# Kernel optimization log

Measured on AMD Instinct MI355X. Metric: run time of the kernel, lower is better.

## Reference

```python
import jax, jax.numpy as jnp
import numpy as np

B, T, D, H, E = 4, 2048, 768, 3072, 8


def setup_inputs() -> dict:
    key = jax.random.key(0)
    ks = jax.random.split(key, 7)
    s_d = 1.0 / np.sqrt(D)
    s_h = 1.0 / np.sqrt(H)
    return {
        "x": jax.random.normal(ks[0], (B, T, D), dtype=jnp.float32),
        # gate: Linear(D, E). (Original inits to zero; random here for nontrivial routing.)
        "Wg": jax.random.normal(ks[1], (E, D), dtype=jnp.float32) * s_d,
        "bg": jax.random.normal(ks[2], (E,), dtype=jnp.float32) * 0.01,
        # stacked expert MLPs: Linear(D,H) -> GELU(exact) -> Linear(H,D)
        "W1": jax.random.normal(ks[3], (E, D, H), dtype=jnp.float32) * s_d,
        "b1": jax.random.normal(ks[4], (E, H), dtype=jnp.float32) * s_d,
        "W2": jax.random.normal(ks[5], (E, H, D), dtype=jnp.float32) * s_h,
        "b2": jax.random.normal(ks[6], (E, D), dtype=jnp.float32) * s_h,
    }


def reference(x, Wg, bg, W1, b1, W2, b2):
    b, t, d = x.shape
    xf = x.reshape(-1, d)                      # [N, D]
    n = xf.shape[0]
    logits = xf @ Wg.T + bg                    # [N, E]
    probs = jax.nn.softmax(logits, axis=-1)
    top2_vals, top2_idx = jax.lax.top_k(probs, 2)  # [N, 2]
    # combine weights: cw[n, e] = top2 prob if expert e is in token n's top-2 else 0
    cw = jnp.zeros((n, Wg.shape[0]), dtype=x.dtype)
    cw = cw.at[jnp.arange(n)[:, None], top2_idx].set(top2_vals)
    # per-expert MLP on all tokens (zero combine weight kills non-routed experts)
    h = jax.nn.gelu(jnp.einsum('nd,edh->neh', xf, W1) + b1[None], approximate=False)
    y = jnp.einsum('neh,ehd->ned', h, W2) + b2[None]   # [N, E, D]
    out = jnp.einsum('ne,ned->nd', cw, y)
    return out.reshape(b, t, d)
```

## Files before the change

kernel.cpp:

```cpp
#include <hip/hip_runtime.h>
#include <hip/hip_bf16.h>
#include <math.h>

#define E_EXPERTS 8
#define D_DIM 768
#define H_DIM 3072
#define N_TOK 8192
#define SLOTS (2 * N_TOK)
#define SCAT_BLOCKS 32
#define MB_L 20

typedef unsigned short ushort_t;
typedef __attribute__((ext_vector_type(8))) __bf16 bf16x8;
typedef __attribute__((ext_vector_type(4))) float f32x4;

__device__ __forceinline__ unsigned short f2bf(float f) {
    unsigned int u = __float_as_uint(f);
    unsigned int r = (u + 0x7FFFu + ((u >> 16) & 1u)) >> 16;
    return (unsigned short)r;
}

__device__ __forceinline__ void gload_lds16(const void* g, void* l) {
    __builtin_amdgcn_global_load_lds(
        (const __attribute__((address_space(1))) unsigned int*)g,
        (__attribute__((address_space(3))) unsigned int*)l, 16, 0, 0);
}


__global__ void transpose_conv_kernel(const float* __restrict__ src, ushort_t* __restrict__ dst,
                                      int R, int C) {
    __shared__ float tile[64][65];
    int e = blockIdx.z;
    const float* S = src + (size_t)e * R * C;
    ushort_t* Dp = dst + (size_t)e * R * C;
    int c0 = blockIdx.x * 64, r0 = blockIdx.y * 64;
    int tx = threadIdx.x & 15, ty = threadIdx.x >> 4;
#pragma unroll
    for (int p = 0; p < 4; p++) {
        float4 v = *(const float4*)&S[(size_t)(r0 + ty + 16 * p) * C + c0 + tx * 4];
        tile[ty + 16 * p][tx * 4 + 0] = v.x;
        tile[ty + 16 * p][tx * 4 + 1] = v.y;
        tile[ty + 16 * p][tx * 4 + 2] = v.z;
        tile[ty + 16 * p][tx * 4 + 3] = v.w;
    }
    __syncthreads();
#pragma unroll
    for (int p = 0; p < 4; p++) {
        int cc = ty + 16 * p;
        int rr = tx * 4;
        ushort4 o;
        o.x = f2bf(tile[rr + 0][cc]);
        o.y = f2bf(tile[rr + 1][cc]);
        o.z = f2bf(tile[rr + 2][cc]);
        o.w = f2bf(tile[rr + 3][cc]);
        *(ushort4*)&Dp[(size_t)(c0 + cc) * R + r0 + rr] = o;
    }
}


__global__ void gate_kernel(const float* __restrict__ x, const float* __restrict__ Wg,
                            const float* __restrict__ bg, ushort_t* __restrict__ xb,
                            int* __restrict__ top_idx, float* __restrict__ top_w) {
    int w = threadIdx.x >> 6, lane = threadIdx.x & 63;
    int t = blockIdx.x * 4 + w;
    if (t >= N_TOK) return;
    const float* xr = x + (size_t)t * D_DIM;
    float xs[12];
#pragma unroll
    for (int j = 0; j < 12; j++) xs[j] = xr[lane + 64 * j];
#pragma unroll
    for (int j = 0; j < 12; j++) xb[(size_t)t * D_DIM + lane + 64 * j] = f2bf(xs[j]);
    float pr[8];
#pragma unroll
    for (int ee = 0; ee < 8; ee++) {
        const float* wr = Wg + ee * D_DIM;
        float p = 0.f;
#pragma unroll
        for (int j = 0; j < 12; j++) p += xs[j] * wr[lane + 64 * j];
#pragma unroll
        for (int o = 32; o > 0; o >>= 1) p += __shfl_xor(p, o);
        pr[ee] = p + bg[ee];
    }
    float mx = pr[0];
#pragma unroll
    for (int ee = 1; ee < 8; ee++) mx = fmaxf(mx, pr[ee]);
    float s = 0.f;
#pragma unroll
    for (int ee = 0; ee < 8; ee++) { pr[ee] = expf(pr[ee] - mx); s += pr[ee]; }
    float inv = 1.f / s;
#pragma unroll
    for (int ee = 0; ee < 8; ee++) pr[ee] *= inv;
    int i0 = 0;
#pragma unroll
    for (int ee = 1; ee < 8; ee++) if (pr[ee] > pr[i0]) i0 = ee;
    int i1 = -1;
#pragma unroll
    for (int ee = 0; ee < 8; ee++) {
        if (ee == i0) continue;
        if (i1 < 0 || pr[ee] > pr[i1]) i1 = ee;
    }
    if (lane == 0) {
        top_idx[2 * t] = i0;
        top_idx[2 * t + 1] = i1;
        top_w[2 * t] = pr[i0];
        top_w[2 * t + 1] = pr[i1];
    }
}

__global__ void hist_kernel(const int* __restrict__ top_idx, int* __restrict__ bc) {
    __shared__ int h[E_EXPERTS];
    if (threadIdx.x < E_EXPERTS) h[threadIdx.x] = 0;
    __syncthreads();
    int t = blockIdx.x * 256 + threadIdx.x;
    atomicAdd(&h[top_idx[2 * t]], 1);
    atomicAdd(&h[top_idx[2 * t + 1]], 1);
    __syncthreads();
    if (threadIdx.x < E_EXPERTS) bc[blockIdx.x * E_EXPERTS + threadIdx.x] = h[threadIdx.x];
}

__global__ void scan_kernel(const int* __restrict__ bc, int* __restrict__ counts,
                            int* __restrict__ offsets, int* __restrict__ base) {
    int tid = threadIdx.x;
    if (tid < E_EXPERTS) {
        int acc = 0;
        for (int b = 0; b < SCAT_BLOCKS; b++) {
            base[b * E_EXPERTS + tid] = acc;
            acc += bc[b * E_EXPERTS + tid];
        }
        counts[tid] = acc;
    }
    __syncthreads();
    if (tid == 0) {
        int acc = 0;
        for (int e = 0; e < E_EXPERTS; e++) { offsets[e] = acc; acc += counts[e]; }
    }
    __syncthreads();
    if (tid < E_EXPERTS) {
        int o = offsets[tid];
        for (int b = 0; b < SCAT_BLOCKS; b++) base[b * E_EXPERTS + tid] += o;
    }
}

__global__ void scatter_kernel(const int* __restrict__ top_idx, const float* __restrict__ top_w,
                               const int* __restrict__ base, int* __restrict__ perm,
                               float* __restrict__ wgt, int* __restrict__ tok2slot) {
    __shared__ int cur[E_EXPERTS];
    if (threadIdx.x < E_EXPERTS) cur[threadIdx.x] = 0;
    __syncthreads();
    int t = blockIdx.x * 256 + threadIdx.x;
#pragma unroll
    for (int sl = 0; sl < 2; sl++) {
        int ee = top_idx[2 * t + sl];
        int p = atomicAdd(&cur[ee], 1);
        int s = base[blockIdx.x * E_EXPERTS + ee] + p;
        perm[s] = t;
        wgt[s] = top_w[2 * t + sl];
        tok2slot[2 * t + sl] = s;
    }
}

__global__ void combine_kernel(const float* __restrict__ y, const int* __restrict__ tok2slot,
                               float* __restrict__ out) {
    int idx = blockIdx.x * blockDim.x + threadIdx.x;
    int stride = gridDim.x * blockDim.x;
    const int QR = D_DIM / 4;
    for (int i = idx; i < N_TOK * QR; i += stride) {
        int t = i / QR, d4 = i - t * QR;
        int s0 = tok2slot[2 * t], s1 = tok2slot[2 * t + 1];
        float4 a = ((const float4*)(y + (size_t)s0 * D_DIM))[d4];
        float4 b = ((const float4*)(y + (size_t)s1 * D_DIM))[d4];
        float4 o;
        o.x = a.x + b.x; o.y = a.y + b.y; o.z = a.z + b.z; o.w = a.w + b.w;
        ((float4*)(out + (size_t)t * D_DIM))[d4] = o;
    }
}

template <int MODE>
__global__ __launch_bounds__(256, 3) void moe_gemm_kernel(
    const ushort_t* __restrict__ A, const ushort_t* __restrict__ BT,
    const float* __restrict__ bias, const int* __restrict__ offsets,
    const int* __restrict__ counts, const int* __restrict__ perm,
    const float* __restrict__ wgt, ushort_t* __restrict__ Hout, float* __restrict__ Y) {
    constexpr int K = (MODE == 0) ? D_DIM : H_DIM;
    constexpr int N = (MODE == 0) ? H_DIM : D_DIM;
    constexpr int KT = K / 32;
    constexpr int NB = N / 128;

    const int wgid = blockIdx.x;
    const int c = wgid & 7;
    const int r = wgid >> 3;
    const int mb = r % MB_L;
    const int q = r / MB_L;
    const int g = q * 8 + c;
    const int e = g / NB;
    const int nb = g % NB;

    const int ne = counts[e];
    const int m0 = mb * 128;
    if (m0 >= ne) return;
    const int n0 = nb * 128;
    const int base = offsets[e];
    const ushort_t* Bt = BT + (size_t)e * ((size_t)N * K);

    __shared__ alignas(16) ushort_t As[3 * 128 * 32];
    __shared__ alignas(16) ushort_t Bs[3 * 128 * 32];

    const int tid = threadIdx.x;
    const int lane = tid & 63;
    const int w = tid >> 6;
    const int wm = w >> 1, wn = w & 1;
    const int lr = lane & 15;
    const int gq = lane >> 4;

    int lds_dst[2];
    int a_src[2], b_src[2];
#pragma unroll
    for (int i = 0; i < 2; i++) {
        int s = 2 * w + i;
        int row = s * 16 + (lane >> 2);
        int lg = ((lane & 3) - (row >> 1)) & 3;
        int rcl = min(m0 + row, ne - 1);
        int arow = (MODE == 0) ? perm[base + rcl] : (base + rcl);
        a_src[i] = arow * K + lg * 8;
        b_src[i] = (n0 + row) * K + lg * 8;
        lds_dst[i] = s * 512;
    }

    auto stage = [&](int tt, int bi) {
#pragma unroll
        for (int i = 0; i < 2; i++) {
            gload_lds16(A + (size_t)a_src[i] + (size_t)tt * 32, &As[bi * 4096 + lds_dst[i]]);
            gload_lds16(Bt + (size_t)b_src[i] + (size_t)tt * 32, &Bs[bi * 4096 + lds_dst[i]]);
        }
    };

    f32x4 acc[4][4];
#pragma unroll
    for (int i = 0; i < 4; i++)
#pragma unroll
        for (int j = 0; j < 4; j++) acc[i][j] = (f32x4){0.f, 0.f, 0.f, 0.f};

    stage(0, 0);
    stage(1, 1);
    asm volatile("s_waitcnt vmcnt(4)" ::: "memory");
    __builtin_amdgcn_s_barrier();

    int cur = 0;
    for (int t = 0; t < KT; ++t) {
        int sb = cur + 2; if (sb >= 3) sb -= 3;
        if (t + 2 < KT) stage(t + 2, sb);
        bf16x8 af[4], bfr[4];
#pragma unroll
        for (int f = 0; f < 4; f++) {
            int Ra = wm * 64 + f * 16 + lr;
            int Rb = wn * 64 + f * 16 + lr;
            af[f]  = *(const bf16x8*)&As[cur * 4096 + Ra * 32 + (((gq + (Ra >> 1)) & 3) << 3)];
            bfr[f] = *(const bf16x8*)&Bs[cur * 4096 + Rb * 32 + (((gq + (Rb >> 1)) & 3) << 3)];
        }
        asm volatile("s_waitcnt lgkmcnt(0)" ::: "memory");
        __builtin_amdgcn_s_setprio(1);
#pragma unroll
        for (int fm = 0; fm < 4; fm++)
#pragma unroll
            for (int fc = 0; fc < 4; fc++)
                acc[fm][fc] = __builtin_amdgcn_mfma_f32_16x16x32_bf16(
                    af[fm], bfr[fc], acc[fm][fc], 0, 0, 0);
        __builtin_amdgcn_s_setprio(0);
        if (t + 2 < KT) asm volatile("s_waitcnt vmcnt(4)" ::: "memory");
        else            asm volatile("s_waitcnt vmcnt(0)" ::: "memory");
        __builtin_amdgcn_s_barrier();
        cur = (cur == 2) ? 0 : cur + 1;
    }

    const int rg0 = gq * 4;
#pragma unroll
    for (int fr = 0; fr < 4; fr++) {
#pragma unroll
        for (int fc = 0; fc < 4; fc++) {
            int cn = n0 + wn * 64 + fc * 16 + lr;
            float bi = bias[e * N + cn];
            f32x4 v = acc[fr][fc];
#pragma unroll
            for (int rg = 0; rg < 4; rg++) {
                int rm = m0 + wm * 64 + fr * 16 + rg0 + rg;
                if (rm < ne) {
                    if (MODE == 0) {
                        float xv = v[rg] + bi;
                        float u = xv * 1.5957691216f * __builtin_fmaf(0.044715f * xv, xv, 1.0f);
                        float gl = xv / (1.f + __expf(-u));
                        Hout[(size_t)(base + rm) * H_DIM + cn] = f2bf(gl);
                    } else {
                        int s = base + rm;
                        float wv = wgt[s];
                        Y[(size_t)s * D_DIM + cn] = wv * (v[rg] + bi);
                    }
                }
            }
        }
    }
}


extern "C" void kernel_launch(void* const* d_in, const int* in_sizes, int n_in,
                              void* d_out, int out_size, void* d_ws, size_t ws_size,
                              hipStream_t stream) {
    const float* x  = (const float*)d_in[0];
    const float* Wg = (const float*)d_in[1];
    const float* bg = (const float*)d_in[2];
    const float* W1 = (const float*)d_in[3];
    const float* b1 = (const float*)d_in[4];
    const float* W2 = (const float*)d_in[5];
    const float* b2 = (const float*)d_in[6];
    float* out = (float*)d_out;

    char* p = (char*)d_ws;
    ushort_t* xb  = (ushort_t*)p; p += (size_t)N_TOK * D_DIM * 2;
    ushort_t* W1T = (ushort_t*)p; p += (size_t)E_EXPERTS * H_DIM * D_DIM * 2;
    ushort_t* W2T = (ushort_t*)p; p += (size_t)E_EXPERTS * D_DIM * H_DIM * 2;
    ushort_t* Hb  = (ushort_t*)p; p += (size_t)SLOTS * H_DIM * 2;
    int*   top_idx = (int*)p;   p += (size_t)N_TOK * 2 * 4;
    float* top_w   = (float*)p; p += (size_t)N_TOK * 2 * 4;
    int*   perm    = (int*)p;   p += (size_t)SLOTS * 4;
    float* wgt     = (float*)p; p += (size_t)SLOTS * 4;
    int*   t2s     = (int*)p;   p += (size_t)SLOTS * 4;
    int*   bc      = (int*)p;   p += SCAT_BLOCKS * E_EXPERTS * 4;
    int*   basep   = (int*)p;   p += SCAT_BLOCKS * E_EXPERTS * 4;
    int*   counts  = (int*)p;   p += 64;
    int*   offsets = (int*)p;   p += 64;
    float* y = (float*)d_ws;

    gate_kernel<<<N_TOK / 4, 256, 0, stream>>>(x, Wg, bg, xb, top_idx, top_w);
    transpose_conv_kernel<<<dim3(H_DIM / 64, D_DIM / 64, E_EXPERTS), 256, 0, stream>>>(W1, W1T, D_DIM, H_DIM);
    transpose_conv_kernel<<<dim3(D_DIM / 64, H_DIM / 64, E_EXPERTS), 256, 0, stream>>>(W2, W2T, H_DIM, D_DIM);
    hist_kernel<<<SCAT_BLOCKS, 256, 0, stream>>>(top_idx, bc);
    scan_kernel<<<1, 64, 0, stream>>>(bc, counts, offsets, basep);
    scatter_kernel<<<SCAT_BLOCKS, 256, 0, stream>>>(top_idx, top_w, basep, perm, wgt, t2s);
    moe_gemm_kernel<0><<<8 * MB_L * (H_DIM / 128), 256, 0, stream>>>(
        xb, W1T, b1, offsets, counts, perm, wgt, Hb, nullptr);
    moe_gemm_kernel<1><<<8 * MB_L * (D_DIM / 128), 256, 0, stream>>>(
        Hb, W2T, b2, offsets, counts, perm, wgt, nullptr, y);
    combine_kernel<<<2048, 256, 0, stream>>>(y, t2s, out);
}
```

Measured before the change: 395.4 us.

## Widen MoE GEMM tiles to 128x256 with 8 waves and add nontemporal stores

```diff
diff --git a/kernel.cpp b/kernel.cpp
--- a/kernel.cpp
+++ b/kernel.cpp
@@ -167,16 +167,15 @@
     for (int i = idx; i < N_TOK * QR; i += stride) {
         int t = i / QR, d4 = i - t * QR;
         int s0 = tok2slot[2 * t], s1 = tok2slot[2 * t + 1];
-        float4 a = ((const float4*)(y + (size_t)s0 * D_DIM))[d4];
-        float4 b = ((const float4*)(y + (size_t)s1 * D_DIM))[d4];
-        float4 o;
-        o.x = a.x + b.x; o.y = a.y + b.y; o.z = a.z + b.z; o.w = a.w + b.w;
-        ((float4*)(out + (size_t)t * D_DIM))[d4] = o;
+        f32x4 a = __builtin_nontemporal_load((const f32x4*)(y + (size_t)s0 * D_DIM) + d4);
+        f32x4 b = __builtin_nontemporal_load((const f32x4*)(y + (size_t)s1 * D_DIM) + d4);
+        f32x4 o = a + b;
+        __builtin_nontemporal_store(o, (f32x4*)(out + (size_t)t * D_DIM) + d4);
     }
 }
 
 template <int MODE>
-__global__ __launch_bounds__(256, 3) void moe_gemm_kernel(
+__global__ __launch_bounds__(512, 4) void moe_gemm_kernel(
     const ushort_t* __restrict__ A, const ushort_t* __restrict__ BT,
     const float* __restrict__ bias, const int* __restrict__ offsets,
     const int* __restrict__ counts, const int* __restrict__ perm,
@@ -184,7 +183,7 @@
     constexpr int K = (MODE == 0) ? D_DIM : H_DIM;
     constexpr int N = (MODE == 0) ? H_DIM : D_DIM;
     constexpr int KT = K / 32;
-    constexpr int NB = N / 128;
+    constexpr int NB = N / 256;
 
     const int wgid = blockIdx.x;
     const int c = wgid & 7;
@@ -198,40 +197,44 @@
     const int ne = counts[e];
     const int m0 = mb * 128;
     if (m0 >= ne) return;
-    const int n0 = nb * 128;
+    const int n0 = nb * 256;
     const int base = offsets[e];
     const ushort_t* Bt = BT + (size_t)e * ((size_t)N * K);
 
     __shared__ alignas(16) ushort_t As[3 * 128 * 32];
-    __shared__ alignas(16) ushort_t Bs[3 * 128 * 32];
+    __shared__ alignas(16) ushort_t Bs[3 * 256 * 32];
 
     const int tid = threadIdx.x;
     const int lane = tid & 63;
     const int w = tid >> 6;
-    const int wm = w >> 1, wn = w & 1;
+    const int wm = w >> 2, wn = w & 3;
     const int lr = lane & 15;
     const int gq = lane >> 4;
 
-    int lds_dst[2];
-    int a_src[2], b_src[2];
-#pragma unroll
-    for (int i = 0; i < 2; i++) {
-        int s = 2 * w + i;
-        int row = s * 16 + (lane >> 2);
-        int lg = ((lane & 3) - (row >> 1)) & 3;
-        int rcl = min(m0 + row, ne - 1);
+    const int lrow = lane >> 2;
+    const int lpg = lane & 3;
+    int a_src, b_src[2];
+    {
+        int rowA = w * 16 + lrow;
+        int lgA = (lpg - (rowA >> 1)) & 3;
+        int rcl = min(m0 + rowA, ne - 1);
         int arow = (MODE == 0) ? perm[base + rcl] : (base + rcl);
-        a_src[i] = arow * K + lg * 8;
-        b_src[i] = (n0 + row) * K + lg * 8;
-        lds_dst[i] = s * 512;
+        a_src = arow * K + lgA * 8;
+#pragma unroll
+        for (int i = 0; i < 2; i++) {
+            int s = 2 * w + i;
+            int rowB = s * 16 + lrow;
+            int lgB = (lpg - (rowB >> 1)) & 3;
+            b_src[i] = (n0 + rowB) * K + lgB * 8;
+        }
     }
 
     auto stage = [&](int tt, int bi) {
-#pragma unroll
-        for (int i = 0; i < 2; i++) {
-            gload_lds16(A + (size_t)a_src[i] + (size_t)tt * 32, &As[bi * 4096 + lds_dst[i]]);
-            gload_lds16(Bt + (size_t)b_src[i] + (size_t)tt * 32, &Bs[bi * 4096 + lds_dst[i]]);
-        }
+        gload_lds16(A + (size_t)a_src + (size_t)tt * 32, &As[bi * 4096 + w * 512]);
+#pragma unroll
+        for (int i = 0; i < 2; i++)
+            gload_lds16(Bt + (size_t)b_src[i] + (size_t)tt * 32,
+                        &Bs[bi * 8192 + (2 * w + i) * 512]);
     };
 
     f32x4 acc[4][4];
@@ -242,7 +245,7 @@
 
     stage(0, 0);
     stage(1, 1);
-    asm volatile("s_waitcnt vmcnt(4)" ::: "memory");
+    asm volatile("s_waitcnt vmcnt(3)" ::: "memory");
     __builtin_amdgcn_s_barrier();
 
     int cur = 0;
@@ -255,7 +258,7 @@
             int Ra = wm * 64 + f * 16 + lr;
             int Rb = wn * 64 + f * 16 + lr;
             af[f]  = *(const bf16x8*)&As[cur * 4096 + Ra * 32 + (((gq + (Ra >> 1)) & 3) << 3)];
-            bfr[f] = *(const bf16x8*)&Bs[cur * 4096 + Rb * 32 + (((gq + (Rb >> 1)) & 3) << 3)];
+            bfr[f] = *(const bf16x8*)&Bs[cur * 8192 + Rb * 32 + (((gq + (Rb >> 1)) & 3) << 3)];
         }
         asm volatile("s_waitcnt lgkmcnt(0)" ::: "memory");
         __builtin_amdgcn_s_setprio(1);
@@ -266,7 +269,7 @@
                 acc[fm][fc] = __builtin_amdgcn_mfma_f32_16x16x32_bf16(
                     af[fm], bfr[fc], acc[fm][fc], 0, 0, 0);
         __builtin_amdgcn_s_setprio(0);
-        if (t + 2 < KT) asm volatile("s_waitcnt vmcnt(4)" ::: "memory");
+        if (t + 2 < KT) asm volatile("s_waitcnt vmcnt(3)" ::: "memory");
         else            asm volatile("s_waitcnt vmcnt(0)" ::: "memory");
         __builtin_amdgcn_s_barrier();
         cur = (cur == 2) ? 0 : cur + 1;
@@ -288,11 +291,13 @@
                         float xv = v[rg] + bi;
                         float u = xv * 1.5957691216f * __builtin_fmaf(0.044715f * xv, xv, 1.0f);
                         float gl = xv / (1.f + __expf(-u));
-                        Hout[(size_t)(base + rm) * H_DIM + cn] = f2bf(gl);
+                        __builtin_nontemporal_store(
+                            f2bf(gl), &Hout[(size_t)(base + rm) * H_DIM + cn]);
                     } else {
                         int s = base + rm;
                         float wv = wgt[s];
-                        Y[(size_t)s * D_DIM + cn] = wv * (v[rg] + bi);
+                        __builtin_nontemporal_store(
+                            wv * (v[rg] + bi), &Y[(size_t)s * D_DIM + cn]);
                     }
                 }
             }
@@ -335,9 +340,9 @@
     hist_kernel<<<SCAT_BLOCKS, 256, 0, stream>>>(top_idx, bc);
     scan_kernel<<<1, 64, 0, stream>>>(bc, counts, offsets, basep);
     scatter_kernel<<<SCAT_BLOCKS, 256, 0, stream>>>(top_idx, top_w, basep, perm, wgt, t2s);
-    moe_gemm_kernel<0><<<8 * MB_L * (H_DIM / 128), 256, 0, stream>>>(
+    moe_gemm_kernel<0><<<8 * MB_L * (H_DIM / 256), 512, 0, stream>>>(
         xb, W1T, b1, offsets, counts, perm, wgt, Hb, nullptr);
-    moe_gemm_kernel<1><<<8 * MB_L * (D_DIM / 128), 256, 0, stream>>>(
+    moe_gemm_kernel<1><<<8 * MB_L * (D_DIM / 256), 512, 0, stream>>>(
         Hb, W2T, b2, offsets, counts, perm, wgt, nullptr, y);
     combine_kernel<<<2048, 256, 0, stream>>>(y, t2s, out);
 }
```

After: 378.7 us. -4.2%, faster.

## Use single-buffered 64-wide K tiles with XOR swizzle in MoE GEMM

Applied to the files above, without the earlier changes.

```diff
diff --git a/kernel.cpp b/kernel.cpp
--- a/kernel.cpp
+++ b/kernel.cpp
@@ -167,11 +167,10 @@
     for (int i = idx; i < N_TOK * QR; i += stride) {
         int t = i / QR, d4 = i - t * QR;
         int s0 = tok2slot[2 * t], s1 = tok2slot[2 * t + 1];
-        float4 a = ((const float4*)(y + (size_t)s0 * D_DIM))[d4];
-        float4 b = ((const float4*)(y + (size_t)s1 * D_DIM))[d4];
-        float4 o;
-        o.x = a.x + b.x; o.y = a.y + b.y; o.z = a.z + b.z; o.w = a.w + b.w;
-        ((float4*)(out + (size_t)t * D_DIM))[d4] = o;
+        f32x4 a = __builtin_nontemporal_load((const f32x4*)(y + (size_t)s0 * D_DIM) + d4);
+        f32x4 b = __builtin_nontemporal_load((const f32x4*)(y + (size_t)s1 * D_DIM) + d4);
+        f32x4 o = a + b;
+        __builtin_nontemporal_store(o, (f32x4*)(out + (size_t)t * D_DIM) + d4);
     }
 }
 
@@ -183,7 +182,7 @@
     const float* __restrict__ wgt, ushort_t* __restrict__ Hout, float* __restrict__ Y) {
     constexpr int K = (MODE == 0) ? D_DIM : H_DIM;
     constexpr int N = (MODE == 0) ? H_DIM : D_DIM;
-    constexpr int KT = K / 32;
+    constexpr int KT = K / 64;
     constexpr int NB = N / 128;
 
     const int wgid = blockIdx.x;
@@ -202,77 +201,72 @@
     const int base = offsets[e];
     const ushort_t* Bt = BT + (size_t)e * ((size_t)N * K);
 
-    __shared__ alignas(16) ushort_t As[3 * 128 * 32];
-    __shared__ alignas(16) ushort_t Bs[3 * 128 * 32];
+    __shared__ alignas(16) ushort_t As[128 * 64];
+    __shared__ alignas(16) ushort_t Bs[128 * 64];
 
     const int tid = threadIdx.x;
     const int lane = tid & 63;
     const int w = tid >> 6;
     const int wm = w >> 1, wn = w & 1;
     const int lr = lane & 15;
-    const int gq = lane >> 4;
-
-    int lds_dst[2];
-    int a_src[2], b_src[2];
-#pragma unroll
-    for (int i = 0; i < 2; i++) {
-        int s = 2 * w + i;
-        int row = s * 16 + (lane >> 2);
-        int lg = ((lane & 3) - (row >> 1)) & 3;
+    const int lk8 = lane >> 4;
+
+    const int trow = tid >> 3;
+    const int sg8 = (((tid & 7) ^ (trow & 7)) * 8);
+    int a_off[4], b_off[4];
+#pragma unroll
+    for (int i = 0; i < 4; i++) {
+        int row = i * 32 + trow;
         int rcl = min(m0 + row, ne - 1);
         int arow = (MODE == 0) ? perm[base + rcl] : (base + rcl);
-        a_src[i] = arow * K + lg * 8;
-        b_src[i] = (n0 + row) * K + lg * 8;
-        lds_dst[i] = s * 512;
-    }
-
-    auto stage = [&](int tt, int bi) {
-#pragma unroll
-        for (int i = 0; i < 2; i++) {
-            gload_lds16(A + (size_t)a_src[i] + (size_t)tt * 32, &As[bi * 4096 + lds_dst[i]]);
-            gload_lds16(Bt + (size_t)b_src[i] + (size_t)tt * 32, &Bs[bi * 4096 + lds_dst[i]]);
+        a_off[i] = arow * K + sg8;
+        b_off[i] = (n0 + row) * K + sg8;
+    }
+
+    auto stage = [&](int tt) {
+#pragma unroll
+        for (int i = 0; i < 4; i++)
+            gload_lds16(A + (size_t)a_off[i] + (size_t)tt * 64, &As[(i * 256 + w * 64) * 8]);
+#pragma unroll
+        for (int i = 0; i < 4; i++)
+            gload_lds16(Bt + (size_t)b_off[i] + (size_t)tt * 64, &Bs[(i * 256 + w * 64) * 8]);
+    };
+
+    f32x4 acc[4][4];
+#pragma unroll
+    for (int i = 0; i < 4; i++)
+#pragma unroll
+        for (int j = 0; j < 4; j++) acc[i][j] = (f32x4){0.f, 0.f, 0.f, 0.f};
+
+    const int cg0 = ((0 * 4 + lk8) ^ (lr & 7)) << 3;
+    const int cg1 = ((1 * 4 + lk8) ^ (lr & 7)) << 3;
+
+    stage(0);
+    for (int t = 0; t < KT; ++t) {
+        __syncthreads();
+        bf16x8 bfr[4][2];
+#pragma unroll
+        for (int fc = 0; fc < 4; fc++) {
+            int Rb = (wn * 64 + fc * 16 + lr) * 64;
+            bfr[fc][0] = *(const bf16x8*)&Bs[Rb + cg0];
+            bfr[fc][1] = *(const bf16x8*)&Bs[Rb + cg1];
         }
-    };
-
-    f32x4 acc[4][4];
-#pragma unroll
-    for (int i = 0; i < 4; i++)
-#pragma unroll
-        for (int j = 0; j < 4; j++) acc[i][j] = (f32x4){0.f, 0.f, 0.f, 0.f};
-
-    stage(0, 0);
-    stage(1, 1);
-    asm volatile("s_waitcnt vmcnt(4)" ::: "memory");
-    __builtin_amdgcn_s_barrier();
-
-    int cur = 0;
-    for (int t = 0; t < KT; ++t) {
-        int sb = cur + 2; if (sb >= 3) sb -= 3;
-        if (t + 2 < KT) stage(t + 2, sb);
-        bf16x8 af[4], bfr[4];
-#pragma unroll
-        for (int f = 0; f < 4; f++) {
-            int Ra = wm * 64 + f * 16 + lr;
-            int Rb = wn * 64 + f * 16 + lr;
-            af[f]  = *(const bf16x8*)&As[cur * 4096 + Ra * 32 + (((gq + (Ra >> 1)) & 3) << 3)];
-            bfr[f] = *(const bf16x8*)&Bs[cur * 4096 + Rb * 32 + (((gq + (Rb >> 1)) & 3) << 3)];
+#pragma unroll
+        for (int pl = 0; pl < 4; pl++) {
+            int Ra = (wm * 64 + pl * 16 + lr) * 64;
+            bf16x8 a0 = *(const bf16x8*)&As[Ra + cg0];
+            bf16x8 a1 = *(const bf16x8*)&As[Ra + cg1];
+#pragma unroll
+            for (int fc = 0; fc < 4; fc++) {
+                acc[pl][fc] = __builtin_amdgcn_mfma_f32_16x16x32_bf16(a0, bfr[fc][0], acc[pl][fc], 0, 0, 0);
+                acc[pl][fc] = __builtin_amdgcn_mfma_f32_16x16x32_bf16(a1, bfr[fc][1], acc[pl][fc], 0, 0, 0);
+            }
         }
-        asm volatile("s_waitcnt lgkmcnt(0)" ::: "memory");
-        __builtin_amdgcn_s_setprio(1);
-#pragma unroll
-        for (int fm = 0; fm < 4; fm++)
-#pragma unroll
-            for (int fc = 0; fc < 4; fc++)
-                acc[fm][fc] = __builtin_amdgcn_mfma_f32_16x16x32_bf16(
-                    af[fm], bfr[fc], acc[fm][fc], 0, 0, 0);
-        __builtin_amdgcn_s_setprio(0);
-        if (t + 2 < KT) asm volatile("s_waitcnt vmcnt(4)" ::: "memory");
-        else            asm volatile("s_waitcnt vmcnt(0)" ::: "memory");
-        __builtin_amdgcn_s_barrier();
-        cur = (cur == 2) ? 0 : cur + 1;
-    }
-
-    const int rg0 = gq * 4;
+        __syncthreads();
+        if (t + 1 < KT) stage(t + 1);
+    }
+
+    const int rg0 = lk8 * 4;
 #pragma unroll
     for (int fr = 0; fr < 4; fr++) {
 #pragma unroll
```

New measurement: 337.3 us. 14.7% less time.
